# Kernel tuning notes

Hardware: AMD Instinct MI355X
Metric: run time of the kernel (lower is better)

## Reference

```python
import jax, jax.numpy as jnp
import numpy as np

DIM = 1024
NUM_HEADS = 16
HEAD_DIM = DIM // NUM_HEADS
SCALE = HEAD_DIM ** -0.5


def setup_inputs() -> dict:
    key = jax.random.key(0)
    ks = jax.random.split(key, 5)
    x = jax.random.normal(ks[0], (8, 1024, DIM), dtype=jnp.float32)
    # nn.Linear default init ~ U(-1/sqrt(fan_in), 1/sqrt(fan_in)); use scaled normals
    w_qkv = jax.random.normal(ks[1], (DIM, 3 * DIM), dtype=jnp.float32) * (DIM ** -0.5)
    b_qkv = jax.random.normal(ks[2], (3 * DIM,), dtype=jnp.float32) * 0.02
    w_proj = jax.random.normal(ks[3], (DIM, DIM), dtype=jnp.float32) * (DIM ** -0.5)
    b_proj = jax.random.normal(ks[4], (DIM,), dtype=jnp.float32) * 0.02
    return {"x": x, "w_qkv": w_qkv, "b_qkv": b_qkv, "w_proj": w_proj, "b_proj": b_proj}


def reference(x, w_qkv, b_qkv, w_proj, b_proj):
    B, N, D = x.shape
    qkv = x @ w_qkv + b_qkv                       # [B, N, 3D]
    qkv = qkv.reshape(B, N, 3, NUM_HEADS, HEAD_DIM)
    qkv = jnp.transpose(qkv, (2, 0, 3, 1, 4))     # [3, B, H, N, hd]
    q, k, v = qkv[0], qkv[1], qkv[2]
    attn = jnp.einsum('bhqd,bhkd->bhqk', q, k) * SCALE
    attn = jax.nn.softmax(attn, axis=-1)
    out = jnp.einsum('bhqk,bhkd->bhqd', attn, v)  # [B, H, N, hd]
    out = jnp.transpose(out, (0, 2, 1, 3)).reshape(B, N, D)
    out = out @ w_proj + b_proj
    return out
```

## Files before the change

kernel.cpp:

```cpp
#include <hip/hip_runtime.h>
#include <stdint.h>


typedef short bf16x8 __attribute__((ext_vector_type(8)));
typedef float f32x4 __attribute__((ext_vector_type(4)));
typedef uint32_t u32x2 __attribute__((ext_vector_type(2)));

__device__ __forceinline__ short f32_bf16(float f) {
  uint32_t u = __builtin_bit_cast(uint32_t, f);
  u += 0x7FFFu + ((u >> 16) & 1u);
  return (short)(u >> 16);
}

__device__ __forceinline__ float exp2_fast(float x) {
  float r; asm("v_exp_f32 %0, %1" : "=v"(r) : "v"(x)); return r;
}

__device__ __forceinline__ uint32_t cvt_pk_bf16(float lo, float hi) {
  uint32_t r;
  asm("v_cvt_pk_bf16_f32 %0, %1, %2" : "=v"(r) : "v"(lo), "v"(hi));
  return r;
}

__device__ __forceinline__ void gload_lds16(const void* g, void* l) {
  __builtin_amdgcn_global_load_lds(
      (const __attribute__((address_space(1))) uint32_t*)g,
      (__attribute__((address_space(3))) uint32_t*)l, 16, 0, 0);
}

__global__ __launch_bounds__(256) void prep_kernel(
    const float* __restrict__ x, short* __restrict__ xb,
    const float* __restrict__ w_qkv, short* __restrict__ wqkvT,
    const float* __restrict__ w_proj, short* __restrict__ wprojT) {
  __shared__ float tile[64][65];
  const int bx = blockIdx.x, tid = threadIdx.x;
  if (bx < 4096) {
    const int i = bx * 256 + tid;
    const float4 f0 = ((const float4*)x)[i * 2];
    const float4 f1 = ((const float4*)x)[i * 2 + 1];
    bf16x8 o;
    o[0] = f32_bf16(f0.x); o[1] = f32_bf16(f0.y);
    o[2] = f32_bf16(f0.z); o[3] = f32_bf16(f0.w);
    o[4] = f32_bf16(f1.x); o[5] = f32_bf16(f1.y);
    o[6] = f32_bf16(f1.z); o[7] = f32_bf16(f1.w);
    ((bf16x8*)xb)[i] = o;
    return;
  }
  const float* w; short* wt; int N, n0, k0;
  if (bx < 4864) {
    const int b = bx - 4096;
    w = w_qkv; wt = wqkvT; N = 3072; n0 = (b % 48) * 64; k0 = (b / 48) * 64;
  } else {
    const int b = bx - 4864;
    w = w_proj; wt = wprojT; N = 1024; n0 = (b % 16) * 64; k0 = (b / 16) * 64;
  }
  const int tr = tid >> 6, tc = tid & 63;
#pragma unroll
  for (int i = 0; i < 16; ++i) {
    int k = tr + i * 4;
    tile[k][tc] = w[(size_t)(k0 + k) * N + n0 + tc];
  }
  __syncthreads();
#pragma unroll
  for (int i = 0; i < 16; ++i) {
    int a = tr + i * 4;
    wt[(size_t)(n0 + a) * 1024 + k0 + tc] = f32_bf16(tile[tc][a]);
  }
}

template <int EPI>
__global__ __launch_bounds__(256, 4) void gemm4_kernel(
    const short* __restrict__ A, const short* __restrict__ Bt,
    const float* __restrict__ bias, short* __restrict__ Qb,
    short* __restrict__ Kb, short* __restrict__ Vt, float* __restrict__ out,
    int NTN) {
  __shared__ short Asm[128 * 64];
  __shared__ short Bsm[128 * 64];

  const int tid = threadIdx.x;
  const int lane = tid & 63;
  const int w = tid >> 6;
  const int wr = w >> 1, wc = w & 1;
  const int c = lane & 15, g = lane >> 4;

  const int nwg = gridDim.x;
  const int wg = (blockIdx.x & 7) * (nwg >> 3) + (blockIdx.x >> 3);
  const int tm = wg / NTN, tn = wg % NTN;
  const int m0 = tm * 128, n0 = tn * 128;

  f32x4 acc[4][4] = {};

  auto stage = [&](int kk0) {
#pragma unroll
    for (int ci = 0; ci < 4; ++ci) {
      const int p = ci * 256 + tid;
      const int r = p >> 3, s = p & 7;
      gload_lds16(A + (size_t)(m0 + r) * 1024 + kk0 + ((s ^ (r & 7)) * 8),
                  &Asm[p * 8]);
    }
#pragma unroll
    for (int ci = 0; ci < 4; ++ci) {
      const int p = ci * 256 + tid;
      const int r = p >> 3, s = p & 7;
      gload_lds16(Bt + (size_t)(n0 + r) * 1024 + kk0 + ((s ^ (r & 7)) * 8),
                  &Bsm[p * 8]);
    }
  };

  for (int t = 0; t < 16; ++t) {
    stage(t * 64);
    asm volatile("s_waitcnt vmcnt(0)" ::: "memory");
    __builtin_amdgcn_s_barrier();
    __builtin_amdgcn_sched_barrier(0);

    bf16x8 bfr[4][2];
#pragma unroll
    for (int jn = 0; jn < 4; ++jn) {
      const int S = wc * 64 + jn * 16 + c;
#pragma unroll
      for (int kk = 0; kk < 2; ++kk)
        bfr[jn][kk] = *(const bf16x8*)&Bsm[S * 64 + (((kk * 4 + g) ^ (c & 7)) * 8)];
    }
#pragma unroll
    for (int mq = 0; mq < 2; ++mq) {
      bf16x8 af[2][2];
#pragma unroll
      for (int mm = 0; mm < 2; ++mm) {
        const int R = wr * 64 + (mq * 2 + mm) * 16 + c;
#pragma unroll
        for (int kk = 0; kk < 2; ++kk)
          af[mm][kk] = *(const bf16x8*)&Asm[R * 64 + (((kk * 4 + g) ^ (c & 7)) * 8)];
      }
      asm volatile("s_waitcnt lgkmcnt(0)" ::: "memory");
      __builtin_amdgcn_sched_barrier(0);
      __builtin_amdgcn_s_setprio(1);
#pragma unroll
      for (int mm = 0; mm < 2; ++mm)
#pragma unroll
        for (int jn = 0; jn < 4; ++jn)
#pragma unroll
          for (int kk = 0; kk < 2; ++kk)
            acc[mq * 2 + mm][jn] = __builtin_amdgcn_mfma_f32_16x16x32_bf16(
                af[mm][kk], bfr[jn][kk], acc[mq * 2 + mm][jn], 0, 0, 0);
      __builtin_amdgcn_s_setprio(0);
    }
    __builtin_amdgcn_s_barrier();
    __builtin_amdgcn_sched_barrier(0);
  }

#pragma unroll
  for (int mm = 0; mm < 4; ++mm) {
    const int i_base = m0 + wr * 64 + mm * 16 + 4 * g;
#pragma unroll
    for (int nn = 0; nn < 4; ++nn) {
      const int j = n0 + wc * 64 + nn * 16 + c;
      const float bj = bias[j];
      if (EPI == 0) {
        const int three = j >> 10, rem = j & 1023, h = rem >> 6, d = rem & 63;
        const float sc = (three == 1) ? 0.18033688f : 1.0f;
#pragma unroll
        for (int r = 0; r < 4; ++r) {
          const int i = i_base + r;
          const int bb = i >> 10, nnq = i & 1023;
          const int bh = bb * 16 + h;
          const short bv = f32_bf16((acc[mm][nn][r] + bj) * sc);
          if (three == 0)
            Qb[(size_t)(bh * 1024 + nnq) * 64 + d] = bv;
          else if (three == 1)
            Kb[(size_t)(bh * 1024 + nnq) * 64 + d] = bv;
          else
            Vt[(size_t)(bh * 64 + d) * 1024 + nnq] = bv;
        }
      } else {
#pragma unroll
        for (int r = 0; r < 4; ++r)
          out[(size_t)(i_base + r) * 1024 + j] = acc[mm][nn][r] + bj;
      }
    }
  }
}

__global__ __launch_bounds__(256, 2) void attn_kernel(
    const short* __restrict__ Qb, const short* __restrict__ Kb,
    const short* __restrict__ Vt, short* __restrict__ Ao) {
  __shared__ __align__(16) char smem[25600];
  short* Kf = (short*)smem;
  short* Vf = (short*)(smem + 8192);
  short* Pl = (short*)(smem + 16384);

  const int tid = threadIdx.x, lane = tid & 63, w = tid >> 6;
  const int c = lane & 15, g = lane >> 4;
  const int bh = blockIdx.x >> 3, qb = blockIdx.x & 7;
  const int bb = bh >> 4, h = bh & 15;
  const int q0 = qb * 128 + w * 32;

  bf16x8 qf[2][2];
#pragma unroll
  for (int m = 0; m < 2; ++m)
#pragma unroll
    for (int ks = 0; ks < 2; ++ks)
      qf[m][ks] = *(const bf16x8*)(Qb + (size_t)(bh * 1024 + q0 + m * 16 + c) * 64 + ks * 32 + 8 * g);

  f32x4 o[2][4] = {};
  float mrun[2] = {-3.0e38f, -3.0e38f};
  float lrun[2] = {0.f, 0.f};

  const int row_r = tid >> 2, seg = tid & 3;
  const short* kp = Kb + (size_t)(bh * 1024 + row_r) * 64 + seg * 16;
  const short* vp = Vt + (size_t)(bh * 64 + row_r) * 1024 + seg * 16;
  short *kdst0, *kdst1, *vdst0, *vdst1;
  {
    const int d0a = seg * 16, d0b = seg * 16 + 8;
    const int pa = (row_r >> 4) * 2 + (d0a >> 5);
    const int pb = (row_r >> 4) * 2 + (d0b >> 5);
    const int sa = (row_r & 15) + 16 * ((d0a & 31) >> 3);
    const int sb = (row_r & 15) + 16 * ((d0b & 31) >> 3);
    kdst0 = &Kf[(pa * 64 + sa) * 8]; kdst1 = &Kf[(pb * 64 + sb) * 8];
    vdst0 = &Vf[(pa * 64 + sa) * 8]; vdst1 = &Vf[(pb * 64 + sb) * 8];
  }

  uint32_t* plw = (uint32_t*)(Pl + w * 1152);
  const short* plr = Pl + w * 1152;

  auto compute = [&]() {
#pragma unroll
    for (int m = 0; m < 2; ++m) {
      f32x4 s[4];
#pragma unroll
      for (int kt = 0; kt < 4; ++kt) {
        f32x4 sa = {};
#pragma unroll
        for (int ks = 0; ks < 2; ++ks) {
          bf16x8 kb = *(const bf16x8*)&Kf[((kt * 2 + ks) * 64 + lane) * 8];
          sa = __builtin_amdgcn_mfma_f32_16x16x32_bf16(kb, qf[m][ks], sa, 0, 0, 0);
        }
        s[kt] = sa;
      }
      float vmax = s[0][0];
#pragma unroll
      for (int kt = 0; kt < 4; ++kt)
#pragma unroll
        for (int r = 0; r < 4; ++r) vmax = fmaxf(vmax, s[kt][r]);
      vmax = fmaxf(vmax, __shfl_xor(vmax, 16));
      vmax = fmaxf(vmax, __shfl_xor(vmax, 32));
      if (!__all(vmax <= mrun[m] + 8.0f)) {
        float mnew = fmaxf(mrun[m], vmax);
        float al = exp2_fast(mrun[m] - mnew);
        lrun[m] *= al;
#pragma unroll
        for (int dt = 0; dt < 4; ++dt) o[m][dt] *= al;
        mrun[m] = mnew;
      }
      float rs = 0.f;
#pragma unroll
      for (int kt = 0; kt < 4; ++kt) {
        float p0 = exp2_fast(s[kt][0] - mrun[m]);
        float p1 = exp2_fast(s[kt][1] - mrun[m]);
        float p2 = exp2_fast(s[kt][2] - mrun[m]);
        float p3 = exp2_fast(s[kt][3] - mrun[m]);
        rs += (p0 + p1) + (p2 + p3);
        u32x2 pk;
        pk[0] = cvt_pk_bf16(p0, p1);
        pk[1] = cvt_pk_bf16(p2, p3);
        *(u32x2*)&plw[c * 36 + kt * 8 + 2 * g] = pk;
      }
      rs += __shfl_xor(rs, 16);
      rs += __shfl_xor(rs, 32);
      lrun[m] += rs;
#pragma unroll
      for (int kk = 0; kk < 2; ++kk) {
        bf16x8 pb = *(const bf16x8*)(plr + c * 72 + kk * 32 + 8 * g);
#pragma unroll
        for (int dt = 0; dt < 4; ++dt) {
          bf16x8 vb = *(const bf16x8*)&Vf[((dt * 2 + kk) * 64 + lane) * 8];
          o[m][dt] = __builtin_amdgcn_mfma_f32_16x16x32_bf16(vb, pb, o[m][dt], 0, 0, 0);
        }
      }
    }
  };

  bf16x8 ka0, ka1, va0, va1, kc0, kc1, vc0, vc1;
  ka0 = *(const bf16x8*)(kp);     ka1 = *(const bf16x8*)(kp + 8);
  va0 = *(const bf16x8*)(vp);     va1 = *(const bf16x8*)(vp + 8);

  for (int t = 0; t < 16; t += 2) {
    __syncthreads();
    *(bf16x8*)kdst0 = ka0; *(bf16x8*)kdst1 = ka1;
    *(bf16x8*)vdst0 = va0; *(bf16x8*)vdst1 = va1;
    {
      const short* kpt = kp + (size_t)(t + 1) * 4096;
      const short* vpt = vp + (t + 1) * 64;
      kc0 = *(const bf16x8*)(kpt); kc1 = *(const bf16x8*)(kpt + 8);
      vc0 = *(const bf16x8*)(vpt); vc1 = *(const bf16x8*)(vpt + 8);
    }
    __syncthreads();
    compute();
    __syncthreads();
    *(bf16x8*)kdst0 = kc0; *(bf16x8*)kdst1 = kc1;
    *(bf16x8*)vdst0 = vc0; *(bf16x8*)vdst1 = vc1;
    if (t + 2 < 16) {
      const short* kpt = kp + (size_t)(t + 2) * 4096;
      const short* vpt = vp + (t + 2) * 64;
      ka0 = *(const bf16x8*)(kpt); ka1 = *(const bf16x8*)(kpt + 8);
      va0 = *(const bf16x8*)(vpt); va1 = *(const bf16x8*)(vpt + 8);
    }
    __syncthreads();
    compute();
  }

  __syncthreads();
  float* Osc = (float*)smem + w * (16 * 68);
  const int qrow = lane >> 2, dseg = (lane & 3) << 4;
#pragma unroll
  for (int m = 0; m < 2; ++m) {
    const float inv = 1.0f / lrun[m];
#pragma unroll
    for (int dt = 0; dt < 4; ++dt)
#pragma unroll
      for (int r = 0; r < 4; ++r)
        Osc[c * 68 + dt * 16 + 4 * g + r] = o[m][dt][r] * inv;
#pragma unroll
    for (int j = 0; j < 2; ++j) {
      f32x4 a0 = *(f32x4*)&Osc[qrow * 68 + dseg + j * 8];
      f32x4 a1 = *(f32x4*)&Osc[qrow * 68 + dseg + j * 8 + 4];
      bf16x8 ob;
      ob[0] = f32_bf16(a0[0]); ob[1] = f32_bf16(a0[1]);
      ob[2] = f32_bf16(a0[2]); ob[3] = f32_bf16(a0[3]);
      ob[4] = f32_bf16(a1[0]); ob[5] = f32_bf16(a1[1]);
      ob[6] = f32_bf16(a1[2]); ob[7] = f32_bf16(a1[3]);
      *(bf16x8*)(Ao + (size_t)(bb * 1024 + q0 + m * 16 + qrow) * 1024 + h * 64 + dseg + j * 8) = ob;
    }
    __syncthreads();
  }
}

extern "C" void kernel_launch(void* const* d_in, const int* in_sizes, int n_in,
                              void* d_out, int out_size, void* d_ws, size_t ws_size,
                              hipStream_t stream) {
  const float* x = (const float*)d_in[0];
  const float* w_qkv = (const float*)d_in[1];
  const float* b_qkv = (const float*)d_in[2];
  const float* w_proj = (const float*)d_in[3];
  const float* b_proj = (const float*)d_in[4];
  float* out = (float*)d_out;

  char* ws = (char*)d_ws;
  const size_t XB_OFF = 0;
  const size_t WQKVT_OFF = 16777216;
  const size_t WPROJT_OFF = WQKVT_OFF + 6291456;
  const size_t Q_OFF = WPROJT_OFF + 2097152;
  const size_t K_OFF = Q_OFF + 16777216;
  const size_t VT_OFF = K_OFF + 16777216;
  short* xb = (short*)(ws + XB_OFF);
  short* wqkvT = (short*)(ws + WQKVT_OFF);
  short* wprojT = (short*)(ws + WPROJT_OFF);
  short* Qb = (short*)(ws + Q_OFF);
  short* Kb = (short*)(ws + K_OFF);
  short* Vt = (short*)(ws + VT_OFF);
  short* attn_o = xb;

  prep_kernel<<<dim3(5120), dim3(256), 0, stream>>>(
      x, xb, w_qkv, wqkvT, w_proj, wprojT);
  gemm4_kernel<0><<<dim3(1536), dim3(256), 0, stream>>>(
      xb, wqkvT, b_qkv, Qb, Kb, Vt, nullptr, 24);
  attn_kernel<<<dim3(1024), dim3(256), 0, stream>>>(Qb, Kb, Vt, attn_o);
  gemm4_kernel<1><<<dim3(512), dim3(256), 0, stream>>>(
      attn_o, wprojT, b_proj, nullptr, nullptr, nullptr, out, 8);
}
```

Baseline: 303.0 us.

## Simplify GEMM and load K/V straight from global into registers in attention

The GEMM loses its XOR-swizzled LDS layout, XCD-aware block remapping, setprio and sched barriers, and occupancy drops to 2 waves per SIMD. It becomes a plain load-wait-compute loop. The attention kernel stops staging K/V tiles in LDS with double-buffered register prefetch and instead has each wave load its K and V fragments directly from global memory every iteration. It also remaps blocks so neighbouring blocks fall on different XCDs. Together these remove LDS traffic and barriers in attention, at the cost of redundant global/L2 loads across the four waves, no prefetch overlap, and likely LDS bank conflicts in the unswizzled GEMM.

```diff
diff --git a/kernel.cpp b/kernel.cpp
--- a/kernel.cpp
+++ b/kernel.cpp
@@ -69,91 +69,58 @@
 }
 
 template <int EPI>
-__global__ __launch_bounds__(256, 4) void gemm4_kernel(
+__global__ __launch_bounds__(256, 2) void gemm4_kernel(
     const short* __restrict__ A, const short* __restrict__ Bt,
     const float* __restrict__ bias, short* __restrict__ Qb,
     short* __restrict__ Kb, short* __restrict__ Vt, float* __restrict__ out,
-    int NTN) {
+    int NT) {
   __shared__ short Asm[128 * 64];
   __shared__ short Bsm[128 * 64];
-
   const int tid = threadIdx.x;
   const int lane = tid & 63;
   const int w = tid >> 6;
   const int wr = w >> 1, wc = w & 1;
   const int c = lane & 15, g = lane >> 4;
 
-  const int nwg = gridDim.x;
-  const int wg = (blockIdx.x & 7) * (nwg >> 3) + (blockIdx.x >> 3);
-  const int tm = wg / NTN, tn = wg % NTN;
+  const int tm = blockIdx.x / NT, tn = blockIdx.x % NT;
   const int m0 = tm * 128, n0 = tn * 128;
 
   f32x4 acc[4][4] = {};
 
-  auto stage = [&](int kk0) {
-#pragma unroll
-    for (int ci = 0; ci < 4; ++ci) {
-      const int p = ci * 256 + tid;
-      const int r = p >> 3, s = p & 7;
-      gload_lds16(A + (size_t)(m0 + r) * 1024 + kk0 + ((s ^ (r & 7)) * 8),
-                  &Asm[p * 8]);
-    }
-#pragma unroll
-    for (int ci = 0; ci < 4; ++ci) {
-      const int p = ci * 256 + tid;
-      const int r = p >> 3, s = p & 7;
-      gload_lds16(Bt + (size_t)(n0 + r) * 1024 + kk0 + ((s ^ (r & 7)) * 8),
-                  &Bsm[p * 8]);
-    }
-  };
-
-  for (int t = 0; t < 16; ++t) {
-    stage(t * 64);
+  for (int k0 = 0; k0 < 1024; k0 += 64) {
+#pragma unroll
+    for (int i = 0; i < 4; ++i) {
+      int ch = (w * 4 + i) * 64 + lane;
+      int r = ch >> 3, c8 = ch & 7;
+      gload_lds16(A + (size_t)(m0 + r) * 1024 + k0 + c8 * 8, &Asm[ch * 8]);
+      gload_lds16(Bt + (size_t)(n0 + r) * 1024 + k0 + c8 * 8, &Bsm[ch * 8]);
+    }
     asm volatile("s_waitcnt vmcnt(0)" ::: "memory");
-    __builtin_amdgcn_s_barrier();
-    __builtin_amdgcn_sched_barrier(0);
-
-    bf16x8 bfr[4][2];
-#pragma unroll
-    for (int jn = 0; jn < 4; ++jn) {
-      const int S = wc * 64 + jn * 16 + c;
-#pragma unroll
-      for (int kk = 0; kk < 2; ++kk)
-        bfr[jn][kk] = *(const bf16x8*)&Bsm[S * 64 + (((kk * 4 + g) ^ (c & 7)) * 8)];
-    }
-#pragma unroll
-    for (int mq = 0; mq < 2; ++mq) {
-      bf16x8 af[2][2];
-#pragma unroll
-      for (int mm = 0; mm < 2; ++mm) {
-        const int R = wr * 64 + (mq * 2 + mm) * 16 + c;
-#pragma unroll
-        for (int kk = 0; kk < 2; ++kk)
-          af[mm][kk] = *(const bf16x8*)&Asm[R * 64 + (((kk * 4 + g) ^ (c & 7)) * 8)];
-      }
-      asm volatile("s_waitcnt lgkmcnt(0)" ::: "memory");
-      __builtin_amdgcn_sched_barrier(0);
-      __builtin_amdgcn_s_setprio(1);
-#pragma unroll
-      for (int mm = 0; mm < 2; ++mm)
-#pragma unroll
-        for (int jn = 0; jn < 4; ++jn)
-#pragma unroll
-          for (int kk = 0; kk < 2; ++kk)
-            acc[mq * 2 + mm][jn] = __builtin_amdgcn_mfma_f32_16x16x32_bf16(
-                af[mm][kk], bfr[jn][kk], acc[mq * 2 + mm][jn], 0, 0, 0);
-      __builtin_amdgcn_s_setprio(0);
-    }
-    __builtin_amdgcn_s_barrier();
-    __builtin_amdgcn_sched_barrier(0);
-  }
-
-#pragma unroll
-  for (int mm = 0; mm < 4; ++mm) {
-    const int i_base = m0 + wr * 64 + mm * 16 + 4 * g;
-#pragma unroll
-    for (int nn = 0; nn < 4; ++nn) {
-      const int j = n0 + wc * 64 + nn * 16 + c;
+    __syncthreads();
+#pragma unroll
+    for (int kk = 0; kk < 2; ++kk) {
+      bf16x8 a[4], b[4];
+#pragma unroll
+      for (int m = 0; m < 4; ++m)
+        a[m] = *(const bf16x8*)&Asm[(wr * 64 + m * 16 + c) * 64 + kk * 32 + 8 * g];
+#pragma unroll
+      for (int n = 0; n < 4; ++n)
+        b[n] = *(const bf16x8*)&Bsm[(wc * 64 + n * 16 + c) * 64 + kk * 32 + 8 * g];
+#pragma unroll
+      for (int m = 0; m < 4; ++m)
+#pragma unroll
+        for (int n = 0; n < 4; ++n)
+          acc[m][n] = __builtin_amdgcn_mfma_f32_16x16x32_bf16(a[m], b[n], acc[m][n], 0, 0, 0);
+    }
+    __syncthreads();
+  }
+
+#pragma unroll
+  for (int m = 0; m < 4; ++m) {
+    const int i_base = m0 + wr * 64 + m * 16 + 4 * g;
+#pragma unroll
+    for (int n = 0; n < 4; ++n) {
+      const int j = n0 + wc * 64 + n * 16 + c;
       const float bj = bias[j];
       if (EPI == 0) {
         const int three = j >> 10, rem = j & 1023, h = rem >> 6, d = rem & 63;
@@ -161,36 +128,36 @@
 #pragma unroll
         for (int r = 0; r < 4; ++r) {
           const int i = i_base + r;
-          const int bb = i >> 10, nnq = i & 1023;
+          const int bb = i >> 10, nn = i & 1023;
           const int bh = bb * 16 + h;
-          const short bv = f32_bf16((acc[mm][nn][r] + bj) * sc);
+          const short bv = f32_bf16((acc[m][n][r] + bj) * sc);
           if (three == 0)
-            Qb[(size_t)(bh * 1024 + nnq) * 64 + d] = bv;
+            Qb[(size_t)(bh * 1024 + nn) * 64 + d] = bv;
           else if (three == 1)
-            Kb[(size_t)(bh * 1024 + nnq) * 64 + d] = bv;
+            Kb[(size_t)(bh * 1024 + nn) * 64 + d] = bv;
           else
-            Vt[(size_t)(bh * 64 + d) * 1024 + nnq] = bv;
+            Vt[(size_t)(bh * 64 + d) * 1024 + nn] = bv;
         }
       } else {
 #pragma unroll
         for (int r = 0; r < 4; ++r)
-          out[(size_t)(i_base + r) * 1024 + j] = acc[mm][nn][r] + bj;
-      }
-    }
-  }
-}
-
-__global__ __launch_bounds__(256, 2) void attn_kernel(
+          out[(size_t)(i_base + r) * 1024 + j] = acc[m][n][r] + bj;
+      }
+    }
+  }
+}
+
+__global__ __launch_bounds__(256) void attn_kernel(
     const short* __restrict__ Qb, const short* __restrict__ Kb,
     const short* __restrict__ Vt, short* __restrict__ Ao) {
-  __shared__ __align__(16) char smem[25600];
-  short* Kf = (short*)smem;
-  short* Vf = (short*)(smem + 8192);
-  short* Pl = (short*)(smem + 16384);
+  __shared__ __align__(16) char smem[17408];
+  short* Pl = (short*)smem;
 
   const int tid = threadIdx.x, lane = tid & 63, w = tid >> 6;
   const int c = lane & 15, g = lane >> 4;
-  const int bh = blockIdx.x >> 3, qb = blockIdx.x & 7;
+  const int p = blockIdx.x;
+  const int lg = (p & 7) * 128 + (p >> 3);
+  const int bh = lg >> 3, qb = lg & 7;
   const int bb = bh >> 4, h = bh & 15;
   const int q0 = qb * 128 + w * 32;
 
@@ -205,24 +172,27 @@
   float mrun[2] = {-3.0e38f, -3.0e38f};
   float lrun[2] = {0.f, 0.f};
 
-  const int row_r = tid >> 2, seg = tid & 3;
-  const short* kp = Kb + (size_t)(bh * 1024 + row_r) * 64 + seg * 16;
-  const short* vp = Vt + (size_t)(bh * 64 + row_r) * 1024 + seg * 16;
-  short *kdst0, *kdst1, *vdst0, *vdst1;
-  {
-    const int d0a = seg * 16, d0b = seg * 16 + 8;
-    const int pa = (row_r >> 4) * 2 + (d0a >> 5);
-    const int pb = (row_r >> 4) * 2 + (d0b >> 5);
-    const int sa = (row_r & 15) + 16 * ((d0a & 31) >> 3);
-    const int sb = (row_r & 15) + 16 * ((d0b & 31) >> 3);
-    kdst0 = &Kf[(pa * 64 + sa) * 8]; kdst1 = &Kf[(pb * 64 + sb) * 8];
-    vdst0 = &Vf[(pa * 64 + sa) * 8]; vdst1 = &Vf[(pb * 64 + sb) * 8];
-  }
-
   uint32_t* plw = (uint32_t*)(Pl + w * 1152);
   const short* plr = Pl + w * 1152;
 
-  auto compute = [&]() {
+  const short* kbase0 = Kb + (size_t)bh * 1024 * 64;
+  const short* vbase0 = Vt + (size_t)bh * 64 * 1024;
+
+  for (int t = 0; t < 16; ++t) {
+    const int kv0 = t * 64;
+    bf16x8 kb[4][2];
+#pragma unroll
+    for (int kt = 0; kt < 4; ++kt)
+#pragma unroll
+      for (int ks = 0; ks < 2; ++ks)
+        kb[kt][ks] = *(const bf16x8*)(kbase0 + (size_t)(kv0 + kt * 16 + c) * 64 + ks * 32 + 8 * g);
+    bf16x8 vb[4][2];
+#pragma unroll
+    for (int dt = 0; dt < 4; ++dt)
+#pragma unroll
+      for (int kk = 0; kk < 2; ++kk)
+        vb[dt][kk] = *(const bf16x8*)(vbase0 + (size_t)(dt * 16 + c) * 1024 + kv0 + kk * 32 + 8 * g);
+
 #pragma unroll
     for (int m = 0; m < 2; ++m) {
       f32x4 s[4];
@@ -230,10 +200,8 @@
       for (int kt = 0; kt < 4; ++kt) {
         f32x4 sa = {};
 #pragma unroll
-        for (int ks = 0; ks < 2; ++ks) {
-          bf16x8 kb = *(const bf16x8*)&Kf[((kt * 2 + ks) * 64 + lane) * 8];
-          sa = __builtin_amdgcn_mfma_f32_16x16x32_bf16(kb, qf[m][ks], sa, 0, 0, 0);
-        }
+        for (int ks = 0; ks < 2; ++ks)
+          sa = __builtin_amdgcn_mfma_f32_16x16x32_bf16(kb[kt][ks], qf[m][ks], sa, 0, 0, 0);
         s[kt] = sa;
       }
       float vmax = s[0][0];
@@ -271,44 +239,14 @@
       for (int kk = 0; kk < 2; ++kk) {
         bf16x8 pb = *(const bf16x8*)(plr + c * 72 + kk * 32 + 8 * g);
 #pragma unroll
-        for (int dt = 0; dt < 4; ++dt) {
-          bf16x8 vb = *(const bf16x8*)&Vf[((dt * 2 + kk) * 64 + lane) * 8];
-          o[m][dt] = __builtin_amdgcn_mfma_f32_16x16x32_bf16(vb, pb, o[m][dt], 0, 0, 0);
-        }
-      }
-    }
-  };
-
-  bf16x8 ka0, ka1, va0, va1, kc0, kc1, vc0, vc1;
-  ka0 = *(const bf16x8*)(kp);     ka1 = *(const bf16x8*)(kp + 8);
-  va0 = *(const bf16x8*)(vp);     va1 = *(const bf16x8*)(vp + 8);
-
-  for (int t = 0; t < 16; t += 2) {
-    __syncthreads();
-    *(bf16x8*)kdst0 = ka0; *(bf16x8*)kdst1 = ka1;
-    *(bf16x8*)vdst0 = va0; *(bf16x8*)vdst1 = va1;
-    {
-      const short* kpt = kp + (size_t)(t + 1) * 4096;
-      const short* vpt = vp + (t + 1) * 64;
-      kc0 = *(const bf16x8*)(kpt); kc1 = *(const bf16x8*)(kpt + 8);
-      vc0 = *(const bf16x8*)(vpt); vc1 = *(const bf16x8*)(vpt + 8);
-    }
-    __syncthreads();
-    compute();
-    __syncthreads();
-    *(bf16x8*)kdst0 = kc0; *(bf16x8*)kdst1 = kc1;
-    *(bf16x8*)vdst0 = vc0; *(bf16x8*)vdst1 = vc1;
-    if (t + 2 < 16) {
-      const short* kpt = kp + (size_t)(t + 2) * 4096;
-      const short* vpt = vp + (t + 2) * 64;
-      ka0 = *(const bf16x8*)(kpt); ka1 = *(const bf16x8*)(kpt + 8);
-      va0 = *(const bf16x8*)(vpt); va1 = *(const bf16x8*)(vpt + 8);
-    }
-    __syncthreads();
-    compute();
+        for (int dt = 0; dt < 4; ++dt)
+          o[m][dt] = __builtin_amdgcn_mfma_f32_16x16x32_bf16(vb[dt][kk], pb, o[m][dt], 0, 0, 0);
+      }
+    }
   }
 
   __syncthreads();
+
   float* Osc = (float*)smem + w * (16 * 68);
   const int qrow = lane >> 2, dseg = (lane & 3) << 4;
 #pragma unroll
```

Result: slower. 326.4 us (+7.7%).
